# Optimization experiments

Measured on AMD Instinct MI355X. Metric: run time of the kernel, lower is better.

Reference implementation:

```python
import jax, jax.numpy as jnp
import numpy as np

N_NODES = 100000
N_EDGES = 1600000
DK = 32
OUT_DIM = 32


def setup_inputs() -> dict:
    key = jax.random.key(0)
    ks = jax.random.split(key, 7)
    X = jax.random.normal(ks[0], (N_NODES, DK), dtype=jnp.float32)
    K = jax.random.normal(ks[1], (N_NODES, DK), dtype=jnp.float32)
    V = jax.random.normal(ks[2], (N_NODES, DK), dtype=jnp.float32)
    # output projection (nn.Dense(out_dim)) params
    W_o = jax.random.normal(ks[3], (DK, OUT_DIM), dtype=jnp.float32) / np.sqrt(DK)
    b_o = jnp.zeros((OUT_DIM,), dtype=jnp.float32)
    # sparsity descriptor td: edge list, dst sorted so segment ops see sorted ids
    src = jax.random.randint(ks[4], (N_EDGES,), 0, N_NODES, dtype=jnp.int32)
    dst = jnp.sort(jax.random.randint(ks[5], (N_EDGES,), 0, N_NODES, dtype=jnp.int32))
    return {"X": X, "K": K, "V": V, "W_o": W_o, "b_o": b_o,
            "src": src, "dst": dst, "num_seg": N_NODES}


def reference(X, K, V, W_o, b_o, src, dst, num_seg):
    dk = X.shape[-1]
    # per-edge attention logits: <Q[dst], K[src]> / dk  -> (E,)
    scores = jnp.einsum('ed,ed->e', jnp.take(X, dst, axis=0),
                        jnp.take(K, src, axis=0)) / dk
    # segment (per-neighborhood) softmax over edges sharing a dst node
    seg_max = jax.ops.segment_max(scores, dst, num_segments=num_seg,
                                  indices_are_sorted=True)
    e = jnp.exp(scores - jnp.take(seg_max, dst))
    denom = jax.ops.segment_sum(e, dst, num_segments=num_seg,
                                indices_are_sorted=True)
    alpha = e / jnp.take(denom, dst)  # (E,)
    # weighted aggregation of values, scattered back to nodes -> (N, dk)
    agg = jax.ops.segment_sum(alpha[:, None] * jnp.take(V, src, axis=0), dst,
                              num_segments=num_seg, indices_are_sorted=True)
    # output projection W_o
    return agg @ W_o + b_o
```

## Files before the change

### kernel.cpp

```cpp
#include <hip/hip_runtime.h>
#include <math.h>

#define DK 32
#define OUT_DIM 32

typedef float    f32x4 __attribute__((ext_vector_type(4)));
typedef _Float16 h2    __attribute__((ext_vector_type(2)));
typedef _Float16 h8    __attribute__((ext_vector_type(8)));

#if __has_builtin(__builtin_amdgcn_exp2f)
#define EXP2F(x) __builtin_amdgcn_exp2f(x)
#else
#define EXP2F(x) exp2f(x)
#endif

__device__ __forceinline__ h2 as_h2(unsigned u) {
    union { unsigned u; h2 h; } v; v.u = u; return v.h;
}
__device__ __forceinline__ unsigned as_u32(h2 h) {
    union { unsigned u; h2 h; } v; v.h = h; return v.u;
}

__device__ __forceinline__ unsigned q8b(float x, float r) {
    int i = (int)rintf(x * r);
    i = min(127, max(-127, i));
    return (unsigned)(i & 255);
}
__device__ __forceinline__ unsigned pack8x4(float4 f, float r) {
    return q8b(f.x, r) | (q8b(f.y, r) << 8) |
           (q8b(f.z, r) << 16) | (q8b(f.w, r) << 24);
}

__global__ void prep_kernel(const int* __restrict__ dst,
                            const float4* __restrict__ K4,
                            const float4* __restrict__ V4,
                            int E, int N,
                            int* __restrict__ row_ptr,
                            uint2* __restrict__ ROW,
                            unsigned* __restrict__ SC) {
    const int t  = blockIdx.x * blockDim.x + threadIdx.x;
    const int e0 = t * 4;
    if (e0 < E) {
        int cur[4];
        if (e0 + 4 <= E) {
            const int4 dd = *(const int4*)(dst + e0);
            cur[0] = dd.x; cur[1] = dd.y; cur[2] = dd.z; cur[3] = dd.w;
        } else {
#pragma unroll
            for (int k = 0; k < 4; ++k)
                cur[k] = (e0 + k < E) ? dst[e0 + k] : 0;
        }
        int prev = (e0 == 0) ? -1 : dst[e0 - 1];
#pragma unroll
        for (int k = 0; k < 4; ++k) {
            const int ee = e0 + k;
            if (ee < E) {
                for (int j = prev + 1; j <= cur[k]; ++j) row_ptr[j] = ee;
                if (ee == E - 1)
                    for (int j = cur[k] + 1; j <= N; ++j) row_ptr[j] = E;
                prev = cur[k];
            }
        }
    }
    if (t < N) {
        float4 kf[8], vf[8];
#pragma unroll
        for (int u = 0; u < 8; ++u) { kf[u] = K4[t * 8 + u]; vf[u] = V4[t * 8 + u]; }
        float mk = 0.0f, mv = 0.0f;
#pragma unroll
        for (int u = 0; u < 8; ++u) {
            mk = fmaxf(mk, fmaxf(fmaxf(fabsf(kf[u].x), fabsf(kf[u].y)),
                                 fmaxf(fabsf(kf[u].z), fabsf(kf[u].w))));
            mv = fmaxf(mv, fmaxf(fmaxf(fabsf(vf[u].x), fabsf(vf[u].y)),
                                 fmaxf(fabsf(vf[u].z), fabsf(vf[u].w))));
        }
        const float rk = (mk > 0.0f) ? 127.0f / mk : 0.0f;
        const float rv = (mv > 0.0f) ? 127.0f / mv : 0.0f;
        uint4* o4 = (uint4*)(ROW + t * 8);
#pragma unroll
        for (int u2 = 0; u2 < 4; ++u2) {
            uint4 o;
            o.x = pack8x4(kf[2 * u2],     rk);
            o.y = pack8x4(vf[2 * u2],     rv);
            o.z = pack8x4(kf[2 * u2 + 1], rk);
            o.w = pack8x4(vf[2 * u2 + 1], rv);
            o4[u2] = o;
        }
        h2 s;
        s.x = (_Float16)(mk * (1.0f / 127.0f));
        s.y = (_Float16)(mv * (1.0f / 127.0f));
        SC[t] = as_u32(s);
    }
}

__global__ void build_row_ptr_kernel(const int* __restrict__ dst, int E, int N,
                                     int* __restrict__ row_ptr) {
    int e = blockIdx.x * blockDim.x + threadIdx.x;
    if (e >= E) return;
    int cur  = dst[e];
    int prev = (e == 0) ? -1 : dst[e - 1];
    for (int j = prev + 1; j <= cur; ++j) row_ptr[j] = e;
    if (e == E - 1) {
        for (int j = cur + 1; j <= N; ++j) row_ptr[j] = E;
    }
}

__global__ __launch_bounds__(512, 2) void gat_fused_kernel(
    const float* __restrict__ X, const uint2* __restrict__ ROW,
    const unsigned* __restrict__ SC,
    const float* __restrict__ Wo, const float* __restrict__ bo,
    const int* __restrict__ src, const int* __restrict__ row_ptr,
    float* __restrict__ out, int N) {

    __shared__ uint4 s_part[16 * 17];

    const int tid  = threadIdx.x;
    const int w    = tid >> 6;
    const int lane = tid & 63;
    const int g    = lane >> 3;
    const int c    = lane & 7;

    const int n_blk = blockIdx.x * 8;
    const int n     = n_blk + w;

    if (tid < 136) {
        uint4 z; z.x = 0; z.y = 0; z.z = 0; z.w = 0;
        s_part[136 + tid] = z;
    }

    const int B    = __builtin_amdgcn_readfirstlane(row_ptr[min(n, N)]);
    const int En   = __builtin_amdgcn_readfirstlane(row_ptr[min(n + 1, N)]);
    const int deg  = En - B;
    const int dcap = max(En - 1, 0);
    const int T    = (deg + 7) >> 3;

    const float scale = 0.03125f * 1.44269504f;
    float4 qf = ((const float4*)X)[min(n, N - 1) * 8 + c];
    qf.x *= scale; qf.y *= scale; qf.z *= scale; qf.w *= scale;

    float l = 0.0f;
    f32x4 acc = {0.0f, 0.0f, 0.0f, 0.0f};

    auto step = [&](uint2 rv, unsigned sc, int t) {
        const h2 sch = as_h2(sc);
        const float sK = (float)sch.x;
        const float sV = (float)sch.y;
        const int b0 = (int)(char)(rv.x);
        const int b1 = (int)(char)(rv.x >> 8);
        const int b2 = (int)(char)(rv.x >> 16);
        const int b3 = (int)(char)(rv.x >> 24);
        float p = fmaf(qf.x, (float)b0, fmaf(qf.y, (float)b1,
                  fmaf(qf.z, (float)b2, qf.w * (float)b3)));
        p += __shfl_xor(p, 1);
        p += __shfl_xor(p, 2);
        p += __shfl_xor(p, 4);
        p *= sK;
        const float wt = (t * 8 + g < deg) ? EXP2F(p) : 0.0f;
        l += wt;
        const float wv = wt * sV;
        const int c0 = (int)(char)(rv.y);
        const int c1 = (int)(char)(rv.y >> 8);
        const int c2 = (int)(char)(rv.y >> 16);
        const int c3 = (int)(char)(rv.y >> 24);
        acc.x = fmaf(wv, (float)c0, acc.x);
        acc.y = fmaf(wv, (float)c1, acc.y);
        acc.z = fmaf(wv, (float)c2, acc.z);
        acc.w = fmaf(wv, (float)c3, acc.w);
    };

    if (T > 0) {
        const int base = B + g;
        const int s0 = src[min(base,      dcap)];
        const int s1 = src[min(base + 8,  dcap)];
        const int s2 = src[min(base + 16, dcap)];
        const int s3 = src[min(base + 24, dcap)];
        uint2 r0 = {0, 0}, r1 = {0, 0}, r2 = {0, 0}, r3 = {0, 0};
        unsigned x0 = 0, x1 = 0, x2 = 0, x3 = 0;
        r0 = ROW[s0 * 8 + c];               x0 = SC[s0];
        if (T > 1) { r1 = ROW[s1 * 8 + c];  x1 = SC[s1]; }
        if (T > 2) { r2 = ROW[s2 * 8 + c];  x2 = SC[s2]; }
        if (T > 3) { r3 = ROW[s3 * 8 + c];  x3 = SC[s3]; }

        step(r0, x0, 0);
        if (T > 1) step(r1, x1, 1);
        if (T > 2) step(r2, x2, 2);
        if (T > 3) step(r3, x3, 3);

        for (int t = 4; t < T; ++t) {
            const int sx = src[min(B + t * 8 + g, dcap)];
            step(ROW[sx * 8 + c], SC[sx], t);
        }
    }

    l     += __shfl_xor(l, 8);
    acc.x += __shfl_xor(acc.x, 8);
    acc.y += __shfl_xor(acc.y, 8);
    acc.z += __shfl_xor(acc.z, 8);
    acc.w += __shfl_xor(acc.w, 8);
    l += __shfl_xor(l, 16);
    l += __shfl_xor(l, 32);

    const float inv = (deg > 0) ? (1.0f / l) : 0.0f;
    h2 o01, o23;
    o01.x = (_Float16)(acc.x * inv);  o01.y = (_Float16)(acc.y * inv);
    o23.x = (_Float16)(acc.z * inv);  o23.y = (_Float16)(acc.w * inv);

    if ((g & 1) == 0) {
        unsigned* part32 = (unsigned*)s_part;
        const int off = w * 68 + (g >> 1) * 16 + c * 2;
        part32[off]     = as_u32(o01);
        part32[off + 1] = as_u32(o23);
    }

    __syncthreads();

    if (w == 0) {
        const int quad = lane >> 4;
        const int col  = lane & 15;

        union BF { h8 v; _Float16 u[8]; };
        BF bf0, bf1;
#pragma unroll
        for (int j2 = 0; j2 < 8; ++j2) {
            bf0.u[j2] = (_Float16)Wo[(quad * 8 + j2) * OUT_DIM + col];
            bf1.u[j2] = (_Float16)Wo[(quad * 8 + j2) * OUT_DIM + 16 + col];
        }
        const float bias0 = bo[col];
        const float bias1 = bo[16 + col];

        union AF { uint4 u; h8 v; };
        f32x4 C0 = {bias0, bias0, bias0, bias0};
        f32x4 C1 = {bias1, bias1, bias1, bias1};
#pragma unroll
        for (int cc = 0; cc < 4; ++cc) {
            AF a;
            a.u = s_part[col * 17 + cc * 4 + quad];
            C0 = __builtin_amdgcn_mfma_f32_16x16x32_f16(a.v, bf0.v, C0, 0, 0, 0);
            C1 = __builtin_amdgcn_mfma_f32_16x16x32_f16(a.v, bf1.v, C1, 0, 0, 0);
        }
        if (quad < 2) {
#pragma unroll
            for (int r = 0; r < 4; ++r) {
                const int n2 = n_blk + quad * 4 + r;
                if (n2 < N) {
                    out[n2 * OUT_DIM + col]      = C0[r];
                    out[n2 * OUT_DIM + 16 + col] = C1[r];
                }
            }
        }
    }
}

__global__ __launch_bounds__(256) void gat_node_f32_kernel(
    const float* __restrict__ X, const float* __restrict__ Km,
    const float* __restrict__ Vm, const float* __restrict__ Wo,
    const float* __restrict__ bo, const int* __restrict__ src,
    const int* __restrict__ row_ptr, float* __restrict__ out, int N) {
    const int tid  = threadIdx.x;
    const int wave = tid >> 6;
    const int lane = tid & 63;
    const int g    = lane >> 3;
    const int c    = lane & 7;
    const int j    = lane & 31;
    const int half = lane >> 5;
    const int n = blockIdx.x * 4 + wave;
    if (n >= N) return;
    const int begin = row_ptr[n];
    const int end   = row_ptr[n + 1];
    const float4* X4 = (const float4*)X;
    const float4* K4 = (const float4*)Km;
    const float4* V4 = (const float4*)Vm;
    const float4 q4 = X4[n * 8 + c];
    float  l   = 0.0f;
    float4 acc = make_float4(0.0f, 0.0f, 0.0f, 0.0f);
    for (int e0 = begin; e0 < end; e0 += 16) {
        const int  ea = e0 + g;
        const int  eb = ea + 8;
        const bool va = ea < end;
        const bool vb = eb < end;
        const int sa = src[min(ea, end - 1)];
        const int sb = src[min(eb, end - 1)];
        const float4 ka  = K4[sa * 8 + c];
        const float4 kb  = K4[sb * 8 + c];
        const float4 vva = V4[sa * 8 + c];
        const float4 vvb = V4[sb * 8 + c];
        float pa = fmaf(ka.x, q4.x, fmaf(ka.y, q4.y, fmaf(ka.z, q4.z, ka.w * q4.w)));
        float pb = fmaf(kb.x, q4.x, fmaf(kb.y, q4.y, fmaf(kb.z, q4.z, kb.w * q4.w)));
        pa += __shfl_xor(pa, 1);  pb += __shfl_xor(pb, 1);
        pa += __shfl_xor(pa, 2);  pb += __shfl_xor(pb, 2);
        pa += __shfl_xor(pa, 4);  pb += __shfl_xor(pb, 4);
        const float wa = va ? __expf(pa * 0.03125f) : 0.0f;
        const float wb = vb ? __expf(pb * 0.03125f) : 0.0f;
        l += wa + wb;
        acc.x = fmaf(wa, vva.x, acc.x);  acc.y = fmaf(wa, vva.y, acc.y);
        acc.z = fmaf(wa, vva.z, acc.z);  acc.w = fmaf(wa, vva.w, acc.w);
        acc.x = fmaf(wb, vvb.x, acc.x);  acc.y = fmaf(wb, vvb.y, acc.y);
        acc.z = fmaf(wb, vvb.z, acc.z);  acc.w = fmaf(wb, vvb.w, acc.w);
    }
#pragma unroll
    for (int m = 8; m <= 32; m <<= 1) {
        l     += __shfl_xor(l, m);
        acc.x += __shfl_xor(acc.x, m);
        acc.y += __shfl_xor(acc.y, m);
        acc.z += __shfl_xor(acc.z, m);
        acc.w += __shfl_xor(acc.w, m);
    }
    const float inv = (end > begin) ? (1.0f / l) : 0.0f;
    float ag[4] = {acc.x, acc.y, acc.z, acc.w};
    float s = 0.0f;
#pragma unroll
    for (int k = 0; k < 32; ++k) {
        const float a = __int_as_float(
            __builtin_amdgcn_readlane(__float_as_int(ag[k & 3]), k >> 2));
        s = fmaf(a, Wo[k * OUT_DIM + j], s);
    }
    if (half == 0) {
        out[n * OUT_DIM + j] = fmaf(s, inv, bo[j]);
    }
}

extern "C" void kernel_launch(void* const* d_in, const int* in_sizes, int n_in,
                              void* d_out, int out_size, void* d_ws, size_t ws_size,
                              hipStream_t stream) {
    const float* X  = (const float*)d_in[0];
    const float* Km = (const float*)d_in[1];
    const float* Vm = (const float*)d_in[2];
    const float* Wo = (const float*)d_in[3];
    const float* bo = (const float*)d_in[4];
    const int* src  = (const int*)d_in[5];
    const int* dst  = (const int*)d_in[6];

    const int N = in_sizes[0] / DK;
    const int E = in_sizes[5];

    int* row_ptr = (int*)d_ws;
    const size_t row_off = (((size_t)(N + 1) * 4) + 127) & ~(size_t)127;
    const size_t sc_off  = ((row_off + (size_t)N * 64) + 127) & ~(size_t)127;
    uint2*    ROW = (uint2*)((char*)d_ws + row_off);
    unsigned* SCt = (unsigned*)((char*)d_ws + sc_off);
    const size_t need = sc_off + (size_t)N * 4;
    float* out = (float*)d_out;

    const int tb = 256;

    if (ws_size >= need) {
        const int nE4   = (E + 3) / 4;
        const int prep_n = (nE4 > N) ? nE4 : N;
        prep_kernel<<<(prep_n + tb - 1) / tb, tb, 0, stream>>>(
            dst, (const float4*)Km, (const float4*)Vm, E, N,
            row_ptr, ROW, SCt);
        const int grid = (N + 7) / 8;
        gat_fused_kernel<<<grid, 512, 0, stream>>>(X, ROW, SCt, Wo, bo,
                                                   src, row_ptr, out, N);
    } else {
        build_row_ptr_kernel<<<(E + tb - 1) / tb, tb, 0, stream>>>(dst, E, N, row_ptr);
        const int grid = (N + 3) / 4;
        gat_node_f32_kernel<<<grid, 256, 0, stream>>>(X, Km, Vm, Wo, bo,
                                                      src, row_ptr, out, N);
    }
}
```

Measured before the change: 145.7 us.

## Split fused attention into score and PV kernels with int8 dot4 scoring

Splits the single fused gather kernel into a score kernel and a weighted-value kernel. The score kernel quantizes Q to int8 and uses sdot4 for the logits, then writes per-edge fp16 weights and per-node inverse denominators to workspace. The PV kernel re-gathers src, V and the weights, with V stored as unsigned-offset int8 and the offset bias subtracted after accumulation. This cuts ALU work in the dot product, but adds an extra kernel launch, a second pass over src and row_ptr, and per-edge weight traffic. Quantizing Q also lowers logit precision.

```diff
diff --git a/kernel.cpp b/kernel.cpp
--- a/kernel.cpp
+++ b/kernel.cpp
@@ -21,6 +21,20 @@
     union { unsigned u; h2 h; } v; v.h = h; return v.u;
 }
 
+#if __has_builtin(__builtin_amdgcn_sdot4)
+__device__ __forceinline__ int dot4i8(unsigned a, unsigned b) {
+    return __builtin_amdgcn_sdot4((int)a, (int)b, 0, false);
+}
+#else
+__device__ __forceinline__ int dot4i8(unsigned a, unsigned b) {
+    int s = (int)(char)(a) * (int)(char)(b);
+    s += (int)(char)(a >> 8)  * (int)(char)(b >> 8);
+    s += (int)(char)(a >> 16) * (int)(char)(b >> 16);
+    s += (int)(char)(a >> 24) * (int)(char)(b >> 24);
+    return s;
+}
+#endif
+
 __device__ __forceinline__ unsigned q8b(float x, float r) {
     int i = (int)rintf(x * r);
     i = min(127, max(-127, i));
@@ -29,6 +43,15 @@
 __device__ __forceinline__ unsigned pack8x4(float4 f, float r) {
     return q8b(f.x, r) | (q8b(f.y, r) << 8) |
            (q8b(f.z, r) << 16) | (q8b(f.w, r) << 24);
+}
+__device__ __forceinline__ unsigned q8bu(float x, float r) {
+    int i = (int)rintf(x * r);
+    i = min(127, max(-127, i));
+    return (unsigned)(i + 128);
+}
+__device__ __forceinline__ unsigned pack8x4u(float4 f, float r) {
+    return q8bu(f.x, r) | (q8bu(f.y, r) << 8) |
+           (q8bu(f.z, r) << 16) | (q8bu(f.w, r) << 24);
 }
 
 __global__ void prep_kernel(const int* __restrict__ dst,
@@ -36,7 +59,8 @@
                             const float4* __restrict__ V4,
                             int E, int N,
                             int* __restrict__ row_ptr,
-                            uint2* __restrict__ ROW,
+                            unsigned* __restrict__ K8,
+                            unsigned* __restrict__ V8,
                             unsigned* __restrict__ SC) {
     const int t  = blockIdx.x * blockDim.x + threadIdx.x;
     const int e0 = t * 4;
@@ -76,15 +100,21 @@
         }
         const float rk = (mk > 0.0f) ? 127.0f / mk : 0.0f;
         const float rv = (mv > 0.0f) ? 127.0f / mv : 0.0f;
-        uint4* o4 = (uint4*)(ROW + t * 8);
-#pragma unroll
-        for (int u2 = 0; u2 < 4; ++u2) {
-            uint4 o;
-            o.x = pack8x4(kf[2 * u2],     rk);
-            o.y = pack8x4(vf[2 * u2],     rv);
-            o.z = pack8x4(kf[2 * u2 + 1], rk);
-            o.w = pack8x4(vf[2 * u2 + 1], rv);
-            o4[u2] = o;
+        uint4* ko = (uint4*)(K8 + t * 8);
+        uint4* vo = (uint4*)(V8 + t * 8);
+#pragma unroll
+        for (int u2 = 0; u2 < 2; ++u2) {
+            uint4 ok, ov;
+            ok.x = pack8x4 (kf[4 * u2],     rk);
+            ok.y = pack8x4 (kf[4 * u2 + 1], rk);
+            ok.z = pack8x4 (kf[4 * u2 + 2], rk);
+            ok.w = pack8x4 (kf[4 * u2 + 3], rk);
+            ov.x = pack8x4u(vf[4 * u2],     rv);
+            ov.y = pack8x4u(vf[4 * u2 + 1], rv);
+            ov.z = pack8x4u(vf[4 * u2 + 2], rv);
+            ov.w = pack8x4u(vf[4 * u2 + 3], rv);
+            ko[u2] = ok;
+            vo[u2] = ov;
         }
         h2 s;
         s.x = (_Float16)(mk * (1.0f / 127.0f));
@@ -105,14 +135,11 @@
     }
 }
 
-__global__ __launch_bounds__(512, 2) void gat_fused_kernel(
-    const float* __restrict__ X, const uint2* __restrict__ ROW,
-    const unsigned* __restrict__ SC,
-    const float* __restrict__ Wo, const float* __restrict__ bo,
-    const int* __restrict__ src, const int* __restrict__ row_ptr,
-    float* __restrict__ out, int N) {
-
-    __shared__ uint4 s_part[16 * 17];
+__global__ __launch_bounds__(256) void gat_score_kernel(
+    const float* __restrict__ X, const unsigned* __restrict__ K8,
+    const unsigned* __restrict__ SC, const int* __restrict__ src,
+    const int* __restrict__ row_ptr, unsigned short* __restrict__ wbuf,
+    float* __restrict__ linv, int N) {
 
     const int tid  = threadIdx.x;
     const int w    = tid >> 6;
@@ -120,13 +147,7 @@
     const int g    = lane >> 3;
     const int c    = lane & 7;
 
-    const int n_blk = blockIdx.x * 8;
-    const int n     = n_blk + w;
-
-    if (tid < 136) {
-        uint4 z; z.x = 0; z.y = 0; z.z = 0; z.w = 0;
-        s_part[136 + tid] = z;
-    }
+    const int n = blockIdx.x * 4 + w;
 
     const int B    = __builtin_amdgcn_readfirstlane(row_ptr[min(n, N)]);
     const int En   = __builtin_amdgcn_readfirstlane(row_ptr[min(n + 1, N)]);
@@ -134,38 +155,32 @@
     const int dcap = max(En - 1, 0);
     const int T    = (deg + 7) >> 3;
 
-    const float scale = 0.03125f * 1.44269504f;
-    float4 qf = ((const float4*)X)[min(n, N - 1) * 8 + c];
-    qf.x *= scale; qf.y *= scale; qf.z *= scale; qf.w *= scale;
+    const float4 qf = ((const float4*)X)[min(n, N - 1) * 8 + c];
+    float mq = fmaxf(fmaxf(fabsf(qf.x), fabsf(qf.y)),
+                     fmaxf(fabsf(qf.z), fabsf(qf.w)));
+    mq = fmaxf(mq, __shfl_xor(mq, 1));
+    mq = fmaxf(mq, __shfl_xor(mq, 2));
+    mq = fmaxf(mq, __shfl_xor(mq, 4));
+    const float rq = (mq > 0.0f) ? 127.0f / mq : 0.0f;
+    const unsigned qd = pack8x4(qf, rq);
+    const float cS = mq * (0.03125f * 1.44269504f / 127.0f);
 
     float l = 0.0f;
-    f32x4 acc = {0.0f, 0.0f, 0.0f, 0.0f};
-
-    auto step = [&](uint2 rv, unsigned sc, int t) {
-        const h2 sch = as_h2(sc);
-        const float sK = (float)sch.x;
-        const float sV = (float)sch.y;
-        const int b0 = (int)(char)(rv.x);
-        const int b1 = (int)(char)(rv.x >> 8);
-        const int b2 = (int)(char)(rv.x >> 16);
-        const int b3 = (int)(char)(rv.x >> 24);
-        float p = fmaf(qf.x, (float)b0, fmaf(qf.y, (float)b1,
-                  fmaf(qf.z, (float)b2, qf.w * (float)b3)));
-        p += __shfl_xor(p, 1);
-        p += __shfl_xor(p, 2);
-        p += __shfl_xor(p, 4);
-        p *= sK;
-        const float wt = (t * 8 + g < deg) ? EXP2F(p) : 0.0f;
+
+    auto step = [&](unsigned kd, unsigned sc, int t) {
+        int si = dot4i8(kd, qd);
+        si += __shfl_xor(si, 1);
+        si += __shfl_xor(si, 2);
+        si += __shfl_xor(si, 4);
+        const float sK = (float)as_h2(sc).x;
+        const float p  = (float)si * (sK * cS);
+        const bool valid = (t * 8 + g) < deg;
+        const float wt = valid ? EXP2F(p) : 0.0f;
         l += wt;
-        const float wv = wt * sV;
-        const int c0 = (int)(char)(rv.y);
-        const int c1 = (int)(char)(rv.y >> 8);
-        const int c2 = (int)(char)(rv.y >> 16);
-        const int c3 = (int)(char)(rv.y >> 24);
-        acc.x = fmaf(wv, (float)c0, acc.x);
-        acc.y = fmaf(wv, (float)c1, acc.y);
-        acc.z = fmaf(wv, (float)c2, acc.z);
-        acc.w = fmaf(wv, (float)c3, acc.w);
+        if (valid && c == 0) {
+            h2 hw; hw.x = (_Float16)wt; hw.y = hw.x;
+            wbuf[B + t * 8 + g] = (unsigned short)as_u32(hw);
+        }
     };
 
     if (T > 0) {
@@ -174,36 +189,119 @@
         const int s1 = src[min(base + 8,  dcap)];
         const int s2 = src[min(base + 16, dcap)];
         const int s3 = src[min(base + 24, dcap)];
-        uint2 r0 = {0, 0}, r1 = {0, 0}, r2 = {0, 0}, r3 = {0, 0};
+        unsigned k0 = 0, k1 = 0, k2 = 0, k3 = 0;
         unsigned x0 = 0, x1 = 0, x2 = 0, x3 = 0;
-        r0 = ROW[s0 * 8 + c];               x0 = SC[s0];
-        if (T > 1) { r1 = ROW[s1 * 8 + c];  x1 = SC[s1]; }
-        if (T > 2) { r2 = ROW[s2 * 8 + c];  x2 = SC[s2]; }
-        if (T > 3) { r3 = ROW[s3 * 8 + c];  x3 = SC[s3]; }
-
-        step(r0, x0, 0);
-        if (T > 1) step(r1, x1, 1);
-        if (T > 2) step(r2, x2, 2);
-        if (T > 3) step(r3, x3, 3);
-
+        k0 = K8[s0 * 8 + c];               x0 = SC[s0];
+        if (T > 1) { k1 = K8[s1 * 8 + c];  x1 = SC[s1]; }
+        if (T > 2) { k2 = K8[s2 * 8 + c];  x2 = SC[s2]; }
+        if (T > 3) { k3 = K8[s3 * 8 + c];  x3 = SC[s3]; }
+
+        step(k0, x0, 0);
+        if (T > 1) step(k1, x1, 1);
+        if (T > 2) step(k2, x2, 2);
+        if (T > 3) step(k3, x3, 3);
         for (int t = 4; t < T; ++t) {
             const int sx = src[min(B + t * 8 + g, dcap)];
-            step(ROW[sx * 8 + c], SC[sx], t);
-        }
-    }
-
-    l     += __shfl_xor(l, 8);
+            step(K8[sx * 8 + c], SC[sx], t);
+        }
+    }
+
+    l += __shfl_xor(l, 8);
+    l += __shfl_xor(l, 16);
+    l += __shfl_xor(l, 32);
+    if (lane == 0 && n < N) {
+        linv[n] = (deg > 0) ? (1.0f / l) : 0.0f;
+    }
+}
+
+__global__ __launch_bounds__(512) void gat_pv_kernel(
+    const unsigned* __restrict__ V8, const unsigned* __restrict__ SC,
+    const int* __restrict__ src, const int* __restrict__ row_ptr,
+    const unsigned short* __restrict__ wbuf, const float* __restrict__ linv,
+    const float* __restrict__ Wo, const float* __restrict__ bo,
+    float* __restrict__ out, int N) {
+
+    __shared__ uint4 s_part[16 * 17];
+
+    const int tid  = threadIdx.x;
+    const int w    = tid >> 6;
+    const int lane = tid & 63;
+    const int g    = lane >> 3;
+    const int c    = lane & 7;
+
+    const int n_blk = blockIdx.x * 8;
+    const int n     = n_blk + w;
+
+    if (tid < 136) {
+        uint4 z; z.x = 0; z.y = 0; z.z = 0; z.w = 0;
+        s_part[136 + tid] = z;
+    }
+
+    const int B    = __builtin_amdgcn_readfirstlane(row_ptr[min(n, N)]);
+    const int En   = __builtin_amdgcn_readfirstlane(row_ptr[min(n + 1, N)]);
+    const int deg  = En - B;
+    const int dcap = max(En - 1, 0);
+    const int T    = (deg + 7) >> 3;
+
+    const float inv = linv[min(n, N - 1)];
+
+    f32x4 acc = {0.0f, 0.0f, 0.0f, 0.0f};
+    float sw = 0.0f;
+
+    auto step = [&](unsigned vd, unsigned sc, unsigned short wl, int t) {
+        const bool valid = (t * 8 + g) < deg;
+        const float wf = (float)as_h2((unsigned)wl).x;
+        const float sV = (float)as_h2(sc).y;
+        const float wv = valid ? wf * sV : 0.0f;
+        sw += wv;
+        acc.x = fmaf(wv, (float)(vd & 255u),         acc.x);
+        acc.y = fmaf(wv, (float)((vd >> 8) & 255u),  acc.y);
+        acc.z = fmaf(wv, (float)((vd >> 16) & 255u), acc.z);
+        acc.w = fmaf(wv, (float)(vd >> 24),          acc.w);
+    };
+
+    if (T > 0) {
+        const int base = B + g;
+        const int s0 = src[min(base,      dcap)];
+        const int s1 = src[min(base + 8,  dcap)];
+        const int s2 = src[min(base + 16, dcap)];
+        const int s3 = src[min(base + 24, dcap)];
+        unsigned v0 = 0, v1 = 0, v2 = 0, v3 = 0;
+        unsigned x0 = 0, x1 = 0, x2 = 0, x3 = 0;
+        unsigned short w0 = 0, w1 = 0, w2 = 0, w3 = 0;
+        v0 = V8[s0 * 8 + c];  x0 = SC[s0];  w0 = wbuf[min(base, dcap)];
+        if (T > 1) { v1 = V8[s1 * 8 + c];  x1 = SC[s1];
+                     w1 = wbuf[min(base + 8,  dcap)]; }
+        if (T > 2) { v2 = V8[s2 * 8 + c];  x2 = SC[s2];
+                     w2 = wbuf[min(base + 16, dcap)]; }
+        if (T > 3) { v3 = V8[s3 * 8 + c];  x3 = SC[s3];
+                     w3 = wbuf[min(base + 24, dcap)]; }
+
+        step(v0, x0, w0, 0);
+        if (T > 1) step(v1, x1, w1, 1);
+        if (T > 2) step(v2, x2, w2, 2);
+        if (T > 3) step(v3, x3, w3, 3);
+        for (int t = 4; t < T; ++t) {
+            const int e = B + t * 8 + g;
+            const int sx = src[min(e, dcap)];
+            step(V8[sx * 8 + c], SC[sx], wbuf[min(e, dcap)], t);
+        }
+    }
+
     acc.x += __shfl_xor(acc.x, 8);
     acc.y += __shfl_xor(acc.y, 8);
     acc.z += __shfl_xor(acc.z, 8);
     acc.w += __shfl_xor(acc.w, 8);
-    l += __shfl_xor(l, 16);
-    l += __shfl_xor(l, 32);
-
-    const float inv = (deg > 0) ? (1.0f / l) : 0.0f;
+    sw += __shfl_xor(sw, 8);
+    sw += __shfl_xor(sw, 16);
+    sw += __shfl_xor(sw, 32);
+
+    const float bias = 32.0f * sw;
     h2 o01, o23;
-    o01.x = (_Float16)(acc.x * inv);  o01.y = (_Float16)(acc.y * inv);
-    o23.x = (_Float16)(acc.z * inv);  o23.y = (_Float16)(acc.w * inv);
+    o01.x = (_Float16)((acc.x - bias) * inv);
+    o01.y = (_Float16)((acc.y - bias) * inv);
+    o23.x = (_Float16)((acc.z - bias) * inv);
+    o23.y = (_Float16)((acc.w - bias) * inv);
 
     if ((g & 1) == 0) {
         unsigned* part32 = (unsigned*)s_part;
@@ -334,11 +432,17 @@
     const int E = in_sizes[5];
 
     int* row_ptr = (int*)d_ws;
-    const size_t row_off = (((size_t)(N + 1) * 4) + 127) & ~(size_t)127;
-    const size_t sc_off  = ((row_off + (size_t)N * 64) + 127) & ~(size_t)127;
-    uint2*    ROW = (uint2*)((char*)d_ws + row_off);
+    const size_t k8_off  = (((size_t)(N + 1) * 4) + 127) & ~(size_t)127;
+    const size_t v8_off  = ((k8_off + (size_t)N * 32) + 127) & ~(size_t)127;
+    const size_t sc_off  = ((v8_off + (size_t)N * 32) + 127) & ~(size_t)127;
+    const size_t wb_off  = ((sc_off + (size_t)N * 4) + 127) & ~(size_t)127;
+    const size_t li_off  = ((wb_off + (size_t)E * 2) + 127) & ~(size_t)127;
+    unsigned* K8 = (unsigned*)((char*)d_ws + k8_off);
+    unsigned* V8 = (unsigned*)((char*)d_ws + v8_off);
     unsigned* SCt = (unsigned*)((char*)d_ws + sc_off);
-    const size_t need = sc_off + (size_t)N * 4;
+    unsigned short* wbuf = (unsigned short*)((char*)d_ws + wb_off);
+    float* linv = (float*)((char*)d_ws + li_off);
+    const size_t need = li_off + (size_t)N * 4;
     float* out = (float*)d_out;
 
     const int tb = 256;
@@ -348,10 +452,11 @@
         const int prep_n = (nE4 > N) ? nE4 : N;
         prep_kernel<<<(prep_n + tb - 1) / tb, tb, 0, stream>>>(
             dst, (const float4*)Km, (const float4*)Vm, E, N,
-            row_ptr, ROW, SCt);
-        const int grid = (N + 7) / 8;
-        gat_fused_kernel<<<grid, 512, 0, stream>>>(X, ROW, SCt, Wo, bo,
-                                                   src, row_ptr, out, N);
+            row_ptr, K8, V8, SCt);
+        gat_score_kernel<<<(N + 3) / 4, 256, 0, stream>>>(
+            X, K8, SCt, src, row_ptr, wbuf, linv, N);
+        gat_pv_kernel<<<(N + 7) / 8, 512, 0, stream>>>(
+            V8, SCt, src, row_ptr, wbuf, linv, Wo, bo, out, N);
     } else {
         build_row_ptr_kernel<<<(E + tb - 1) / tb, tb, 0, stream>>>(dst, E, N, row_ptr);
         const int grid = (N + 3) / 4;
```

After: 179.2 us. 23.0% more time.

## Split fused GAT kernel into int8 dot-product edge scoring and aggregation passes

Applied to the files above, without the earlier changes.

Quantizes queries to int8 in the prep pass and adds a per-edge score kernel that computes attention logits with packed int8 dot products, storing fp16 weight and weighted-scale per edge. The aggregation kernel then only gathers int8 V rows and precomputed weights, removing the shuffle-based dot-product reduction from the node loop. This trades an extra launch and an E-sized intermediate buffer write/read for simpler, more parallel per-edge scoring, and adds quantization error on Q and fp16 range risk on unnormalized exponentials.

```diff
diff --git a/kernel.cpp b/kernel.cpp
--- a/kernel.cpp
+++ b/kernel.cpp
@@ -21,6 +21,19 @@
     union { unsigned u; h2 h; } v; v.h = h; return v.u;
 }
 
+#if __has_builtin(__builtin_amdgcn_sdot4)
+#define SDOT4(a, b, c) __builtin_amdgcn_sdot4((int)(a), (int)(b), (c), false)
+#else
+__device__ __forceinline__ int sdot4_sw(unsigned a, unsigned b, int c) {
+    c += (int)(char)(a)        * (int)(char)(b);
+    c += (int)(char)(a >> 8)   * (int)(char)(b >> 8);
+    c += (int)(char)(a >> 16)  * (int)(char)(b >> 16);
+    c += (int)(char)(a >> 24)  * (int)(char)(b >> 24);
+    return c;
+}
+#define SDOT4(a, b, c) sdot4_sw((a), (b), (c))
+#endif
+
 __device__ __forceinline__ unsigned q8b(float x, float r) {
     int i = (int)rintf(x * r);
     i = min(127, max(-127, i));
@@ -34,10 +47,14 @@
 __global__ void prep_kernel(const int* __restrict__ dst,
                             const float4* __restrict__ K4,
                             const float4* __restrict__ V4,
+                            const float4* __restrict__ X4,
                             int E, int N,
                             int* __restrict__ row_ptr,
-                            uint2* __restrict__ ROW,
-                            unsigned* __restrict__ SC) {
+                            uint4* __restrict__ K8,
+                            unsigned* __restrict__ V8,
+                            uint4* __restrict__ Q8,
+                            unsigned* __restrict__ SC,
+                            float* __restrict__ SCQ) {
     const int t  = blockIdx.x * blockDim.x + threadIdx.x;
     const int e0 = t * 4;
     if (e0 < E) {
@@ -63,33 +80,51 @@
         }
     }
     if (t < N) {
-        float4 kf[8], vf[8];
-#pragma unroll
-        for (int u = 0; u < 8; ++u) { kf[u] = K4[t * 8 + u]; vf[u] = V4[t * 8 + u]; }
-        float mk = 0.0f, mv = 0.0f;
+        float4 kf[8], vf[8], xf[8];
+#pragma unroll
+        for (int u = 0; u < 8; ++u) {
+            kf[u] = K4[t * 8 + u];
+            vf[u] = V4[t * 8 + u];
+            xf[u] = X4[t * 8 + u];
+        }
+        float mk = 0.0f, mv = 0.0f, mq = 0.0f;
 #pragma unroll
         for (int u = 0; u < 8; ++u) {
             mk = fmaxf(mk, fmaxf(fmaxf(fabsf(kf[u].x), fabsf(kf[u].y)),
                                  fmaxf(fabsf(kf[u].z), fabsf(kf[u].w))));
             mv = fmaxf(mv, fmaxf(fmaxf(fabsf(vf[u].x), fabsf(vf[u].y)),
                                  fmaxf(fabsf(vf[u].z), fabsf(vf[u].w))));
+            mq = fmaxf(mq, fmaxf(fmaxf(fabsf(xf[u].x), fabsf(xf[u].y)),
+                                 fmaxf(fabsf(xf[u].z), fabsf(xf[u].w))));
         }
         const float rk = (mk > 0.0f) ? 127.0f / mk : 0.0f;
         const float rv = (mv > 0.0f) ? 127.0f / mv : 0.0f;
-        uint4* o4 = (uint4*)(ROW + t * 8);
-#pragma unroll
-        for (int u2 = 0; u2 < 4; ++u2) {
-            uint4 o;
-            o.x = pack8x4(kf[2 * u2],     rk);
-            o.y = pack8x4(vf[2 * u2],     rv);
-            o.z = pack8x4(kf[2 * u2 + 1], rk);
-            o.w = pack8x4(vf[2 * u2 + 1], rv);
-            o4[u2] = o;
+        const float rq = (mq > 0.0f) ? 127.0f / mq : 0.0f;
+#pragma unroll
+        for (int u2 = 0; u2 < 2; ++u2) {
+            uint4 ok, oq;
+            ok.x = pack8x4(kf[4 * u2],     rk);
+            ok.y = pack8x4(kf[4 * u2 + 1], rk);
+            ok.z = pack8x4(kf[4 * u2 + 2], rk);
+            ok.w = pack8x4(kf[4 * u2 + 3], rk);
+            oq.x = pack8x4(xf[4 * u2],     rq);
+            oq.y = pack8x4(xf[4 * u2 + 1], rq);
+            oq.z = pack8x4(xf[4 * u2 + 2], rq);
+            oq.w = pack8x4(xf[4 * u2 + 3], rq);
+            K8[t * 2 + u2] = ok;
+            Q8[t * 2 + u2] = oq;
+            uint4 ov;
+            ov.x = pack8x4(vf[4 * u2],     rv);
+            ov.y = pack8x4(vf[4 * u2 + 1], rv);
+            ov.z = pack8x4(vf[4 * u2 + 2], rv);
+            ov.w = pack8x4(vf[4 * u2 + 3], rv);
+            ((uint4*)(V8 + t * 8))[u2] = ov;
         }
         h2 s;
         s.x = (_Float16)(mk * (1.0f / 127.0f));
         s.y = (_Float16)(mv * (1.0f / 127.0f));
-        SC[t] = as_u32(s);
+        SC[t]  = as_u32(s);
+        SCQ[t] = mq * (1.44269504f / (127.0f * 32.0f));
     }
 }
 
@@ -105,11 +140,40 @@
     }
 }
 
-__global__ __launch_bounds__(512, 2) void gat_fused_kernel(
-    const float* __restrict__ X, const uint2* __restrict__ ROW,
-    const unsigned* __restrict__ SC,
+__global__ __launch_bounds__(256) void gat_score_kernel(
+    const uint4* __restrict__ K8, const uint4* __restrict__ Q8,
+    const unsigned* __restrict__ SC, const float* __restrict__ SCQ,
+    const int* __restrict__ src, const int* __restrict__ dst,
+    unsigned* __restrict__ wbuf, int E) {
+    const int e  = blockIdx.x * blockDim.x + threadIdx.x;
+    const int ec = min(e, E - 1);
+    const int s = src[ec];
+    const int d = dst[ec];
+    const uint4 ka = K8[s * 2];
+    const uint4 kb = K8[s * 2 + 1];
+    const uint4 qa = Q8[d * 2];
+    const uint4 qb = Q8[d * 2 + 1];
+    const h2 scv   = as_h2(SC[s]);
+    const float sq = SCQ[d];
+    int si = SDOT4(ka.x, qa.x, 0);
+    si = SDOT4(ka.y, qa.y, si);
+    si = SDOT4(ka.z, qa.z, si);
+    si = SDOT4(ka.w, qa.w, si);
+    si = SDOT4(kb.x, qb.x, si);
+    si = SDOT4(kb.y, qb.y, si);
+    si = SDOT4(kb.z, qb.z, si);
+    si = SDOT4(kb.w, qb.w, si);
+    const float p  = (float)si * ((float)scv.x * sq);
+    const float w  = EXP2F(p);
+    const float wv = w * (float)scv.y;
+    h2 o; o.x = (_Float16)w; o.y = (_Float16)wv;
+    if (e < E) wbuf[e] = as_u32(o);
+}
+
+__global__ __launch_bounds__(512) void gat_pv_kernel(
+    const unsigned* __restrict__ V8, const int* __restrict__ src,
+    const int* __restrict__ row_ptr, const unsigned* __restrict__ wbuf,
     const float* __restrict__ Wo, const float* __restrict__ bo,
-    const int* __restrict__ src, const int* __restrict__ row_ptr,
     float* __restrict__ out, int N) {
 
     __shared__ uint4 s_part[16 * 17];
@@ -134,38 +198,19 @@
     const int dcap = max(En - 1, 0);
     const int T    = (deg + 7) >> 3;
 
-    const float scale = 0.03125f * 1.44269504f;
-    float4 qf = ((const float4*)X)[min(n, N - 1) * 8 + c];
-    qf.x *= scale; qf.y *= scale; qf.z *= scale; qf.w *= scale;
-
     float l = 0.0f;
     f32x4 acc = {0.0f, 0.0f, 0.0f, 0.0f};
 
-    auto step = [&](uint2 rv, unsigned sc, int t) {
-        const h2 sch = as_h2(sc);
-        const float sK = (float)sch.x;
-        const float sV = (float)sch.y;
-        const int b0 = (int)(char)(rv.x);
-        const int b1 = (int)(char)(rv.x >> 8);
-        const int b2 = (int)(char)(rv.x >> 16);
-        const int b3 = (int)(char)(rv.x >> 24);
-        float p = fmaf(qf.x, (float)b0, fmaf(qf.y, (float)b1,
-                  fmaf(qf.z, (float)b2, qf.w * (float)b3)));
-        p += __shfl_xor(p, 1);
-        p += __shfl_xor(p, 2);
-        p += __shfl_xor(p, 4);
-        p *= sK;
-        const float wt = (t * 8 + g < deg) ? EXP2F(p) : 0.0f;
+    auto step = [&](unsigned vd, unsigned wd, int t) {
+        const bool valid = (t * 8 + g) < deg;
+        const h2 wp = as_h2(wd);
+        const float wt = valid ? (float)wp.x : 0.0f;
+        const float wv = valid ? (float)wp.y : 0.0f;
         l += wt;
-        const float wv = wt * sV;
-        const int c0 = (int)(char)(rv.y);
-        const int c1 = (int)(char)(rv.y >> 8);
-        const int c2 = (int)(char)(rv.y >> 16);
-        const int c3 = (int)(char)(rv.y >> 24);
-        acc.x = fmaf(wv, (float)c0, acc.x);
-        acc.y = fmaf(wv, (float)c1, acc.y);
-        acc.z = fmaf(wv, (float)c2, acc.z);
-        acc.w = fmaf(wv, (float)c3, acc.w);
+        acc.x = fmaf(wv, (float)(int)(char)(vd),        acc.x);
+        acc.y = fmaf(wv, (float)(int)(char)(vd >> 8),   acc.y);
+        acc.z = fmaf(wv, (float)(int)(char)(vd >> 16),  acc.z);
+        acc.w = fmaf(wv, (float)(int)(char)(vd >> 24),  acc.w);
     };
 
     if (T > 0) {
@@ -174,29 +219,29 @@
         const int s1 = src[min(base + 8,  dcap)];
         const int s2 = src[min(base + 16, dcap)];
         const int s3 = src[min(base + 24, dcap)];
-        uint2 r0 = {0, 0}, r1 = {0, 0}, r2 = {0, 0}, r3 = {0, 0};
-        unsigned x0 = 0, x1 = 0, x2 = 0, x3 = 0;
-        r0 = ROW[s0 * 8 + c];               x0 = SC[s0];
-        if (T > 1) { r1 = ROW[s1 * 8 + c];  x1 = SC[s1]; }
-        if (T > 2) { r2 = ROW[s2 * 8 + c];  x2 = SC[s2]; }
-        if (T > 3) { r3 = ROW[s3 * 8 + c];  x3 = SC[s3]; }
-
-        step(r0, x0, 0);
-        if (T > 1) step(r1, x1, 1);
-        if (T > 2) step(r2, x2, 2);
-        if (T > 3) step(r3, x3, 3);
-
+        unsigned v0 = 0, v1 = 0, v2 = 0, v3 = 0;
+        unsigned w0 = 0, w1 = 0, w2 = 0, w3 = 0;
+        v0 = V8[s0 * 8 + c];  w0 = wbuf[min(base, dcap)];
+        if (T > 1) { v1 = V8[s1 * 8 + c];  w1 = wbuf[min(base + 8,  dcap)]; }
+        if (T > 2) { v2 = V8[s2 * 8 + c];  w2 = wbuf[min(base + 16, dcap)]; }
+        if (T > 3) { v3 = V8[s3 * 8 + c];  w3 = wbuf[min(base + 24, dcap)]; }
+
+        step(v0, w0, 0);
+        if (T > 1) step(v1, w1, 1);
+        if (T > 2) step(v2, w2, 2);
+        if (T > 3) step(v3, w3, 3);
         for (int t = 4; t < T; ++t) {
-            const int sx = src[min(B + t * 8 + g, dcap)];
-            step(ROW[sx * 8 + c], SC[sx], t);
-        }
-    }
-
-    l     += __shfl_xor(l, 8);
+            const int e = B + t * 8 + g;
+            const int sx = src[min(e, dcap)];
+            step(V8[sx * 8 + c], wbuf[min(e, dcap)], t);
+        }
+    }
+
     acc.x += __shfl_xor(acc.x, 8);
     acc.y += __shfl_xor(acc.y, 8);
     acc.z += __shfl_xor(acc.z, 8);
     acc.w += __shfl_xor(acc.w, 8);
+    l += __shfl_xor(l, 8);
     l += __shfl_xor(l, 16);
     l += __shfl_xor(l, 32);
 
@@ -334,11 +379,19 @@
     const int E = in_sizes[5];
 
     int* row_ptr = (int*)d_ws;
-    const size_t row_off = (((size_t)(N + 1) * 4) + 127) & ~(size_t)127;
-    const size_t sc_off  = ((row_off + (size_t)N * 64) + 127) & ~(size_t)127;
-    uint2*    ROW = (uint2*)((char*)d_ws + row_off);
+    const size_t k8_off  = (((size_t)(N + 1) * 4) + 127) & ~(size_t)127;
+    const size_t v8_off  = ((k8_off + (size_t)N * 32) + 127) & ~(size_t)127;
+    const size_t q8_off  = ((v8_off + (size_t)N * 32) + 127) & ~(size_t)127;
+    const size_t sc_off  = ((q8_off + (size_t)N * 32) + 127) & ~(size_t)127;
+    const size_t sq_off  = ((sc_off + (size_t)N * 4) + 127) & ~(size_t)127;
+    const size_t wb_off  = ((sq_off + (size_t)N * 4) + 127) & ~(size_t)127;
+    uint4*    K8  = (uint4*)((char*)d_ws + k8_off);
+    unsigned* V8  = (unsigned*)((char*)d_ws + v8_off);
+    uint4*    Q8  = (uint4*)((char*)d_ws + q8_off);
     unsigned* SCt = (unsigned*)((char*)d_ws + sc_off);
-    const size_t need = sc_off + (size_t)N * 4;
+    float*    SCQ = (float*)((char*)d_ws + sq_off);
+    unsigned* wbuf = (unsigned*)((char*)d_ws + wb_off);
+    const size_t need = wb_off + (size_t)E * 4;
     float* out = (float*)d_out;
 
     const int tb = 256;
@@ -347,11 +400,12 @@
         const int nE4   = (E + 3) / 4;
         const int prep_n = (nE4 > N) ? nE4 : N;
         prep_kernel<<<(prep_n + tb - 1) / tb, tb, 0, stream>>>(
-            dst, (const float4*)Km, (const float4*)Vm, E, N,
-            row_ptr, ROW, SCt);
-        const int grid = (N + 7) / 8;
-        gat_fused_kernel<<<grid, 512, 0, stream>>>(X, ROW, SCt, Wo, bo,
-                                                   src, row_ptr, out, N);
+            dst, (const float4*)Km, (const float4*)Vm, (const float4*)X,
+            E, N, row_ptr, K8, V8, Q8, SCt, SCQ);
+        gat_score_kernel<<<(E + tb - 1) / tb, tb, 0, stream>>>(
+            K8, Q8, SCt, SCQ, src, dst, wbuf, E);
+        gat_pv_kernel<<<(N + 7) / 8, 512, 0, stream>>>(
+            V8, src, row_ptr, wbuf, Wo, bo, out, N);
     } else {
         build_row_ptr_kernel<<<(E + tb - 1) / tb, tb, 0, stream>>>(dst, E, N, row_ptr);
         const int grid = (N + 3) / 4;
```

After: 160.6 us. +10.3%, slower.
